# Kernel optimization log

Hardware: AMD Instinct MI355X
Metric: run time of the kernel (lower is better)

## Reference

```python
import jax, jax.numpy as jnp
import numpy as np

DIM = 1024
Q_HEADS = 16
KV_HEADS = 4
DIM_HEAD = DIM // Q_HEADS  # 64
SOFTCLAMP = 50.0
EPS = 1e-8


def rotate_half(x):
    x_even = x[..., ::2]
    x_odd = x[..., 1::2]
    return jnp.stack([-x_odd, x_even], axis=-1).reshape(x.shape)


def setup_inputs() -> dict:
    key = jax.random.key(0)
    ks = jax.random.split(key, 10)
    B, S = 1, 2048
    dim_q = DIM_HEAD * Q_HEADS   # 1024
    dim_kv = DIM_HEAD * KV_HEADS  # 256
    std = 0.02
    x = jax.random.normal(ks[0], (B, S, DIM), dtype=jnp.float32)
    positions = jnp.broadcast_to(jnp.arange(S, dtype=jnp.int32)[None, :], (B, S))
    # causal mask: True = disallowed (torch semantics: allowed = ~attn_mask)
    attn_mask = jnp.triu(jnp.ones((S, S), dtype=bool), k=1)
    return {
        "x": x,
        "positions": positions,
        "attn_mask": attn_mask,
        "Wq": jax.random.normal(ks[1], (DIM, dim_q), jnp.float32) * std,
        "Wk": jax.random.normal(ks[2], (DIM, dim_kv), jnp.float32) * std,
        "Wv": jax.random.normal(ks[3], (DIM, dim_kv), jnp.float32) * std,
        "Wo": jax.random.normal(ks[4], (dim_q, DIM), jnp.float32) * std,
        "Wg": jax.random.normal(ks[5], (DIM, Q_HEADS), jnp.float32) * std,
        "Wm": jax.random.normal(ks[6], (DIM, KV_HEADS), jnp.float32) * std,
        "bm": jnp.zeros((KV_HEADS,), jnp.float32),
        "Wvr": jax.random.normal(ks[7], (DIM, dim_kv), jnp.float32) * std,
        "k_scale": jnp.ones((KV_HEADS, DIM_HEAD), jnp.float32),
    }


def reference(x, positions, attn_mask, Wq, Wk, Wv, Wo, Wg, Wm, bm, Wvr, k_scale):
    b, s, _ = x.shape
    h, qh, dh = KV_HEADS, Q_HEADS, DIM_HEAD
    g = qh // h

    q = (x @ Wq).reshape(b, s, qh, dh).transpose(0, 2, 1, 3)  # [b,qh,s,dh]
    k = (x @ Wk).reshape(b, s, h, dh).transpose(0, 2, 1, 3)   # [b,h,s,dh]
    v = (x @ Wv).reshape(b, s, h, dh).transpose(0, 2, 1, 3)

    # value-residual gating: v = lerp(v, residual_v, mix)
    residual_v = (x @ Wvr).reshape(b, s, h, dh).transpose(0, 2, 1, 3)
    mix = jax.nn.sigmoid(x @ Wm + bm).transpose(0, 2, 1)[..., None]  # [b,h,s,1]
    v = v + mix * (residual_v - v)

    # multi-head RMSNorm on k
    rms = jnp.sqrt(jnp.mean(k * k, axis=-1, keepdims=True) + EPS)
    k = k / rms * k_scale[None, :, None, :]

    # rotary embeddings (identical for all heads -> broadcast over head dim)
    inv_freq = 1.0 / (10000.0 ** (jnp.arange(0, dh, 2, dtype=jnp.float32) / dh))
    freqs = positions.astype(jnp.float32)[..., None] * inv_freq  # [b,s,dh/2]
    cos = jnp.repeat(jnp.cos(freqs), 2, axis=-1)[:, None, :, :]  # [b,1,s,dh]
    sin = jnp.repeat(jnp.sin(freqs), 2, axis=-1)[:, None, :, :]
    q = q * cos + rotate_half(q) * sin
    k = k * cos + rotate_half(k) * sin

    # grouped-query attention with softclamped scores
    scale = dh ** -0.5
    qg = q.reshape(b, h, g, s, dh)
    sim = jnp.einsum('bhgqd,bhkd->bhgqk', qg, k) * scale
    sim = jnp.tanh(sim / SOFTCLAMP) * SOFTCLAMP
    allowed = ~attn_mask  # [s,s]
    sim = jnp.where(allowed[None, None, None, :, :], sim, jnp.finfo(sim.dtype).min)
    attn = jax.nn.softmax(sim, axis=-1)
    out = jnp.einsum('bhgqk,bhkd->bhgqd', attn, v).reshape(b, qh, s, dh)

    # per-query-head sigmoid gates
    gates = jax.nn.sigmoid(x @ Wg).transpose(0, 2, 1)[..., None]  # [b,qh,s,1]
    out = out * gates

    out = out.transpose(0, 2, 1, 3).reshape(b, s, qh * dh)
    return out @ Wo
```

## Files before the change

### kernel.cpp

```cpp
#include <hip/hip_runtime.h>
#include <hip/hip_bf16.h>
#include <math.h>

typedef unsigned short u16;
typedef unsigned int u32;
typedef __attribute__((ext_vector_type(8))) __bf16 bf16x8;
typedef __attribute__((ext_vector_type(4))) float f32x4;

__device__ inline u16 f2bf(float f) {
  u32 b = __float_as_uint(f);
  b += 0x7FFFu + ((b >> 16) & 1u);
  return (u16)(b >> 16);
}
__device__ inline float bf2f(u16 b) { return __uint_as_float((u32)b << 16); }

__global__ __launch_bounds__(256) void cvt_bf16_k(
    const float* __restrict__ in, u16* __restrict__ out) {
  int i = (blockIdx.x * 256 + threadIdx.x) * 8;
  float4 v0 = *(const float4*)&in[i];
  float4 v1 = *(const float4*)&in[i + 4];
  uint4 pk;
  pk.x = (u32)f2bf(v0.x) | ((u32)f2bf(v0.y) << 16);
  pk.y = (u32)f2bf(v0.z) | ((u32)f2bf(v0.w) << 16);
  pk.z = (u32)f2bf(v1.x) | ((u32)f2bf(v1.y) << 16);
  pk.w = (u32)f2bf(v1.z) | ((u32)f2bf(v1.w) << 16);
  *(uint4*)&out[i] = pk;
}

__global__ __launch_bounds__(256) void prep_w_k(
    const float* __restrict__ Wq, const float* __restrict__ Wk,
    const float* __restrict__ Wv, const float* __restrict__ Wvr,
    const float* __restrict__ Wo, const float* __restrict__ Wg,
    const float* __restrict__ Wm, u16* __restrict__ WallT,
    u16* __restrict__ WoT) {
  __shared__ float tile[32][33];
  int k0 = blockIdx.x * 32;
  int ybl = blockIdx.y;
  int tx = threadIdx.x, ty = threadIdx.y;
  const float* src;
  int scol, sN, drow;
  u16* dst;
  if (ybl >= 60) {
    src = Wo; scol = (ybl - 60) * 32; sN = 1024; dst = WoT; drow = scol;
  } else {
    int n0 = ybl * 32;
    if (n0 >= 1792) {
#pragma unroll
      for (int j = 0; j < 4; ++j) {
        int n = n0 + ty * 4 + j, j2 = n - 1792, k = k0 + tx;
        float val = (j2 < 16) ? Wg[(size_t)k * 16 + j2]
                  : (j2 < 20) ? Wm[(size_t)k * 4 + (j2 - 16)] : 0.f;
        WallT[(size_t)n * 1024 + k] = f2bf(val);
      }
      return;
    }
    dst = WallT; drow = n0;
    if (n0 < 1024) { src = Wq; scol = n0; sN = 1024; }
    else if (n0 < 1280) { src = Wk; scol = n0 - 1024; sN = 256; }
    else if (n0 < 1536) { src = Wv; scol = n0 - 1280; sN = 256; }
    else { src = Wvr; scol = n0 - 1536; sN = 256; }
  }
#pragma unroll
  for (int j = 0; j < 4; ++j)
    tile[ty * 4 + j][tx] = src[(size_t)(k0 + ty * 4 + j) * sN + scol + tx];
  __syncthreads();
#pragma unroll
  for (int j = 0; j < 4; ++j)
    dst[(size_t)(drow + ty * 4 + j) * 1024 + k0 + tx] = f2bf(tile[tx][ty * 4 + j]);
}

__global__ __launch_bounds__(256) void rope_tab_k(
    const int* __restrict__ positions, float* __restrict__ tab) {
  int idx = blockIdx.x * 256 + threadIdx.x;
  int s = idx >> 5, f = idx & 31;
  float inv = __expf(-(float)f * (9.210340371976184f / 32.f));
  float ang = (float)positions[s] * inv;
  tab[(size_t)s * 64 + f] = cosf(ang);
  tab[(size_t)s * 64 + 32 + f] = sinf(ang);
}

template <int BM, bool BF16_OUT>
__global__ __launch_bounds__(512) void gemm_bf16_k(
    const u16* __restrict__ A, const u16* __restrict__ Bt, void* __restrict__ Cv,
    int M, int N, int K) {
  constexpr int MI = BM / 32;
  __shared__ __align__(16) u16 As[BM * 64];
  __shared__ __align__(16) u16 Bs[128 * 64];
  int tid = threadIdx.x;
  int w = tid >> 6, l = tid & 63;
  int wr = w >> 2, wc = w & 3;
  int lr = l & 15, lg = l >> 4;
  int m0 = blockIdx.y * BM, n0 = blockIdx.x * 128;
  f32x4 zero = {0.f, 0.f, 0.f, 0.f};
  f32x4 acc[MI][2];
#pragma unroll
  for (int mi = 0; mi < MI; ++mi)
#pragma unroll
    for (int ni = 0; ni < 2; ++ni) acc[mi][ni] = zero;

  for (int kt = 0; kt < K; kt += 64) {
    __syncthreads();
#pragma unroll
    for (int c = 0; c < BM * 64 / (8 * 512); ++c) {
      int idx = c * 512 + tid;
      int row = idx >> 3, k0 = (idx & 7) * 8;
      *(uint4*)&As[row * 64 + k0] =
          *(const uint4*)&A[(size_t)(m0 + row) * K + kt + k0];
    }
#pragma unroll
    for (int c = 0; c < 2; ++c) {
      int idx = c * 512 + tid;
      int row = idx >> 3, k0 = (idx & 7) * 8;
      *(uint4*)&Bs[row * 64 + k0] =
          *(const uint4*)&Bt[(size_t)(n0 + row) * K + kt + k0];
    }
    __syncthreads();
#pragma unroll
    for (int kw = 0; kw < 2; ++kw) {
      bf16x8 af[MI], bfr[2];
#pragma unroll
      for (int mi = 0; mi < MI; ++mi)
        af[mi] = *(const bf16x8*)&As[(wr * (BM / 2) + mi * 16 + lr) * 64 + kw * 32 + lg * 8];
#pragma unroll
      for (int ni = 0; ni < 2; ++ni)
        bfr[ni] = *(const bf16x8*)&Bs[(wc * 32 + ni * 16 + lr) * 64 + kw * 32 + lg * 8];
#pragma unroll
      for (int mi = 0; mi < MI; ++mi)
#pragma unroll
        for (int ni = 0; ni < 2; ++ni)
          acc[mi][ni] = __builtin_amdgcn_mfma_f32_16x16x32_bf16(
              af[mi], bfr[ni], acc[mi][ni], 0, 0, 0);
    }
  }
#pragma unroll
  for (int mi = 0; mi < MI; ++mi)
#pragma unroll
    for (int ni = 0; ni < 2; ++ni)
#pragma unroll
      for (int r = 0; r < 4; ++r) {
        int row = m0 + wr * (BM / 2) + mi * 16 + lg * 4 + r;
        int col = n0 + wc * 32 + ni * 16 + lr;
        if (BF16_OUT)
          ((u16*)Cv)[(size_t)row * N + col] = f2bf(acc[mi][ni][r]);
        else
          ((float*)Cv)[(size_t)row * N + col] = acc[mi][ni][r];
      }
}

__global__ __launch_bounds__(256) void postproc_k(
    const float* __restrict__ bm, const float* __restrict__ ksc,
    const float* __restrict__ rtab, u16* __restrict__ qkvrb,
    u16* __restrict__ kb, u16* __restrict__ vb, float* __restrict__ g_out) {
  int s = blockIdx.x, tid = threadIdx.x;
  int lane = tid & 63, w = tid >> 6;
  u16* row = qkvrb + (size_t)s * 1920;
  const float* tr = rtab + (size_t)s * 64;
  if (tid < 16)
    g_out[s * 16 + tid] = 1.f / (1.f + __expf(-bf2f(row[1792 + tid])));
  int h = w, d = lane;
  float c = tr[d >> 1], sn = tr[32 + (d >> 1)];
  {
    float mixv = 1.f / (1.f + __expf(-(bf2f(row[1808 + h]) + bm[h])));
    float vv = bf2f(row[1280 + h * 64 + d]);
    float rv = bf2f(row[1536 + h * 64 + d]);
    vb[((size_t)h * 2048 + s) * 64 + d] = f2bf(vv + mixv * (rv - vv));
  }
  {
    float kv = bf2f(row[1024 + h * 64 + d]);
    float ss = kv * kv;
#pragma unroll
    for (int off = 32; off > 0; off >>= 1) ss += __shfl_xor(ss, off);
    float rms = sqrtf(ss * (1.f / 64.f) + 1e-8f);
    float kn = kv / rms * ksc[h * 64 + d];
    float partner = __shfl_xor(kn, 1);
    kb[((size_t)h * 2048 + s) * 64 + d] =
        f2bf((d & 1) ? fmaf(kn, c, partner * sn) : fmaf(kn, c, -partner * sn));
  }
#pragma unroll
  for (int r = 0; r < 4; ++r) {
    int e = r * 256 + tid;
    int dq = e & 63;
    float cq = tr[dq >> 1], sq = tr[32 + (dq >> 1)];
    float qv = bf2f(row[e]);
    float partner = __shfl_xor(qv, 1);
    float qr = (e & 1) ? fmaf(qv, cq, partner * sq) : fmaf(qv, cq, -partner * sq);
    row[e] = f2bf(qr * 0.125f);
  }
}

#define TPAD 66
__global__ __launch_bounds__(256) void vtrans_k(const u16* __restrict__ vb,
                                               u16* __restrict__ vtb) {
  __shared__ u16 tile[64 * TPAD];
  int h = blockIdx.y, s0 = blockIdx.x * 64;
  int t = threadIdx.x;
  {
    int r = t >> 2, cb = (t & 3) * 16;
    const u16* src = vb + ((size_t)h * 2048 + s0 + r) * 64 + cb;
    *(uint4*)&tile[r * TPAD + cb] = *(const uint4*)src;
    *(uint4*)&tile[r * TPAD + cb + 8] = *(const uint4*)(src + 8);
  }
  __syncthreads();
  int d = t >> 2, sb = (t & 3) * 16;
  u16 vals[16];
#pragma unroll
  for (int j = 0; j < 16; ++j) vals[j] = tile[(sb + j) * TPAD + d];
  uint4 a, b;
  a.x = (u32)vals[0] | ((u32)vals[1] << 16);
  a.y = (u32)vals[2] | ((u32)vals[3] << 16);
  a.z = (u32)vals[4] | ((u32)vals[5] << 16);
  a.w = (u32)vals[6] | ((u32)vals[7] << 16);
  b.x = (u32)vals[8] | ((u32)vals[9] << 16);
  b.y = (u32)vals[10] | ((u32)vals[11] << 16);
  b.z = (u32)vals[12] | ((u32)vals[13] << 16);
  b.w = (u32)vals[14] | ((u32)vals[15] << 16);
  u16* dst = vtb + ((size_t)h * 64 + d) * 2048 + s0 + sb;
  *(uint4*)dst = a;
  *(uint4*)(dst + 8) = b;
}

#define KPAD 72
__global__ __launch_bounds__(256) void attn_k(
    const u16* __restrict__ qkvrb, const u16* __restrict__ kb,
    const u16* __restrict__ vtb, const float* __restrict__ g,
    u16* __restrict__ aob) {
  __shared__ __align__(16) u16 Ks[64 * KPAD];
  __shared__ __align__(16) u16 Vt[64 * KPAD];
  int head = blockIdx.x, hkv = head >> 2;
  int by = blockIdx.y;
  int rb = (by < 16) ? (31 - by) : (by - 16);
  int row0 = rb * 64;
  int tid = threadIdx.x;
  int wi = tid >> 6, l = tid & 63;
  int lr = l & 15, lg = l >> 4;
  int skey = tid >> 2, sdb = (tid & 3) * 16;
  f32x4 zero = {0.f, 0.f, 0.f, 0.f};
  const float C1 = 0.057707801635558534f;
  const float C2 = -144.26950408889634f;
  const u16* qrow = qkvrb + (size_t)(row0 + wi * 16 + lr) * 1920 + head * 64;
  bf16x8 qf0 = *(const bf16x8*)&qrow[lg * 8];
  bf16x8 qf1 = *(const bf16x8*)&qrow[32 + lg * 8];
  f32x4 acc_o[4];
#pragma unroll
  for (int nd = 0; nd < 4; ++nd) acc_o[nd] = zero;
  float l_part = 0.f;
  int qglob = row0 + wi * 16 + lr;
  int src_a = lr + (lg & 1) * 32, src_b = src_a + 16;
  uint4 rk0, rk1, rv0, rv1;
  {
    const u16* kp = kb + ((size_t)hkv * 2048 + skey) * 64 + sdb;
    rk0 = *(const uint4*)kp;
    rk1 = *(const uint4*)(kp + 8);
    const u16* vp = vtb + ((size_t)(hkv * 64 + skey)) * 2048 + sdb;
    rv0 = *(const uint4*)vp;
    rv1 = *(const uint4*)(vp + 8);
  }
#pragma unroll 1
  for (int c = 0; c <= rb; ++c) {
    *(uint4*)&Ks[skey * KPAD + sdb] = rk0;
    *(uint4*)&Ks[skey * KPAD + sdb + 8] = rk1;
    *(uint4*)&Vt[skey * KPAD + sdb] = rv0;
    *(uint4*)&Vt[skey * KPAD + sdb + 8] = rv1;
    __syncthreads();
    if (c < rb) {
      int nb = (c + 1) * 64;
      const u16* kp = kb + ((size_t)hkv * 2048 + nb + skey) * 64 + sdb;
      rk0 = *(const uint4*)kp;
      rk1 = *(const uint4*)(kp + 8);
      const u16* vp = vtb + ((size_t)(hkv * 64 + skey)) * 2048 + nb + sdb;
      rv0 = *(const uint4*)vp;
      rv1 = *(const uint4*)(vp + 8);
    }
    int kbase = c * 64;
    __builtin_amdgcn_s_setprio(1);
    f32x4 sa[4];
#pragma unroll
    for (int ni = 0; ni < 4; ++ni) {
      bf16x8 a0 = *(const bf16x8*)&Ks[(ni * 16 + lr) * KPAD + lg * 8];
      bf16x8 a1 = *(const bf16x8*)&Ks[(ni * 16 + lr) * KPAD + 32 + lg * 8];
      f32x4 t = __builtin_amdgcn_mfma_f32_16x16x32_bf16(a0, qf0, zero, 0, 0, 0);
      sa[ni] = __builtin_amdgcn_mfma_f32_16x16x32_bf16(a1, qf1, t, 0, 0, 0);
    }
    bool diag = (c == rb);
    u32 pkw[4][2];
#pragma unroll
    for (int ni = 0; ni < 4; ++ni) {
      float pv[4];
#pragma unroll
      for (int r = 0; r < 4; ++r) {
        float sv = sa[ni][r];
        float e = __builtin_amdgcn_exp2f(sv * C1);
        float p = __builtin_amdgcn_exp2f(C2 * __builtin_amdgcn_rcpf(e + 1.f));
        if (diag && (kbase + ni * 16 + lg * 4 + r) > qglob) p = 0.f;
        pv[r] = p;
        l_part += p;
      }
      asm("v_cvt_pk_bf16_f32 %0, %1, %2" : "=v"(pkw[ni][0]) : "v"(pv[0]), "v"(pv[1]));
      asm("v_cvt_pk_bf16_f32 %0, %1, %2" : "=v"(pkw[ni][1]) : "v"(pv[2]), "v"(pv[3]));
    }
    union { u32 w[4]; bf16x8 v; } pf0, pf1;
    {
      u32 t0[4], t1[4], t2[4], t3[4];
#define GATHER(T, NI)                          \
      T[0] = __shfl((int)pkw[NI][0], src_a);   \
      T[1] = __shfl((int)pkw[NI][1], src_a);   \
      T[2] = __shfl((int)pkw[NI][0], src_b);   \
      T[3] = __shfl((int)pkw[NI][1], src_b);
      GATHER(t0, 0)
      GATHER(t1, 1)
      GATHER(t2, 2)
      GATHER(t3, 3)
#undef GATHER
      bool hi = (lg & 2) != 0;
#pragma unroll
      for (int kq = 0; kq < 4; ++kq) {
        pf0.w[kq] = hi ? t1[kq] : t0[kq];
        pf1.w[kq] = hi ? t3[kq] : t2[kq];
      }
    }
#pragma unroll
    for (int nd = 0; nd < 4; ++nd) {
      bf16x8 v0 = *(const bf16x8*)&Vt[(nd * 16 + lr) * KPAD + lg * 8];
      bf16x8 v1 = *(const bf16x8*)&Vt[(nd * 16 + lr) * KPAD + 32 + lg * 8];
      acc_o[nd] = __builtin_amdgcn_mfma_f32_16x16x32_bf16(pf0.v, v0, acc_o[nd], 0, 0, 0);
      acc_o[nd] = __builtin_amdgcn_mfma_f32_16x16x32_bf16(pf1.v, v1, acc_o[nd], 0, 0, 0);
    }
    __builtin_amdgcn_s_setprio(0);
    __syncthreads();
  }
  l_part += __shfl_xor(l_part, 16);
  l_part += __shfl_xor(l_part, 32);
#pragma unroll
  for (int r = 0; r < 4; ++r) {
    int row = row0 + wi * 16 + lg * 4 + r;
    float lv = __shfl(l_part, lg * 4 + r);
    float sc = g[row * 16 + head] * __builtin_amdgcn_rcpf(lv);
#pragma unroll
    for (int nd = 0; nd < 4; ++nd)
      aob[(size_t)row * 1024 + head * 64 + nd * 16 + lr] =
          f2bf(acc_o[nd][r] * sc);
  }
}

extern "C" void kernel_launch(void* const* d_in, const int* in_sizes, int n_in,
                              void* d_out, int out_size, void* d_ws,
                              size_t ws_size, hipStream_t stream) {
  const float* x = (const float*)d_in[0];
  const int* positions = (const int*)d_in[1];
  const float* Wq = (const float*)d_in[3];
  const float* Wk = (const float*)d_in[4];
  const float* Wv = (const float*)d_in[5];
  const float* Wo = (const float*)d_in[6];
  const float* Wg = (const float*)d_in[7];
  const float* Wm = (const float*)d_in[8];
  const float* bm = (const float*)d_in[9];
  const float* Wvr = (const float*)d_in[10];
  const float* ksc = (const float*)d_in[11];
  float* out = (float*)d_out;

  u16* xb = (u16*)d_ws;
  u16* WallT = xb + (size_t)2048 * 1024;
  u16* WoT = WallT + (size_t)1920 * 1024;
  u16* qkvrb = WoT + (size_t)1024 * 1024;
  u16* kbuf = qkvrb + (size_t)2048 * 1920;
  u16* vbuf = kbuf + (size_t)4 * 2048 * 64;
  u16* vtb = vbuf + (size_t)4 * 2048 * 64;
  float* gbuf = (float*)(vtb + (size_t)4 * 2048 * 64);
  float* rtab = gbuf + (size_t)2048 * 16;
  u16* aob = xb;

  cvt_bf16_k<<<1024, 256, 0, stream>>>(x, xb);
  prep_w_k<<<dim3(32, 92), dim3(32, 8), 0, stream>>>(Wq, Wk, Wv, Wvr, Wo, Wg,
                                                     Wm, WallT, WoT);
  rope_tab_k<<<256, 256, 0, stream>>>(positions, rtab);
  gemm_bf16_k<128, true><<<dim3(15, 16), 512, 0, stream>>>(xb, WallT, qkvrb,
                                                           2048, 1920, 1024);
  postproc_k<<<2048, 256, 0, stream>>>(bm, ksc, rtab, qkvrb, kbuf, vbuf, gbuf);
  vtrans_k<<<dim3(32, 4), 256, 0, stream>>>(vbuf, vtb);
  attn_k<<<dim3(16, 32), 256, 0, stream>>>(qkvrb, kbuf, vtb, gbuf, aob);
  gemm_bf16_k<64, false><<<dim3(8, 32), 512, 0, stream>>>(aob, WoT, out, 2048,
                                                          1024, 1024);
}
```

Before: 109.0 us.

## Split attention KV loop across two wave groups and pair causal row blocks per workgroup

The attention kernel now runs 512 threads per block, with two groups of four waves each taking alternate KV chunks for the same query rows. The partial outputs and row sums are merged through shared memory before the final write. Each block also handles a long and a short causal row block in sequence, which halves the grid and balances work across blocks. This shortens the serial KV chain per row block, at the cost of extra barriers, a shared-memory reduction, and idle iterations when one group has no chunk left.

```diff
diff --git a/kernel.cpp b/kernel.cpp
--- a/kernel.cpp
+++ b/kernel.cpp
@@ -220,125 +220,152 @@
 }
 
 #define KPAD 72
-__global__ __launch_bounds__(256) void attn_k(
+__global__ __launch_bounds__(512) void attn_k(
     const u16* __restrict__ qkvrb, const u16* __restrict__ kb,
     const u16* __restrict__ vtb, const float* __restrict__ g,
     u16* __restrict__ aob) {
-  __shared__ __align__(16) u16 Ks[64 * KPAD];
-  __shared__ __align__(16) u16 Vt[64 * KPAD];
+  __shared__ __align__(16) u16 smem[18432];
   int head = blockIdx.x, hkv = head >> 2;
-  int by = blockIdx.y;
-  int rb = (by < 16) ? (31 - by) : (by - 16);
-  int row0 = rb * 64;
   int tid = threadIdx.x;
-  int wi = tid >> 6, l = tid & 63;
+  int w = tid >> 6, l = tid & 63;
+  int grp = w >> 2, wi = w & 3;
   int lr = l & 15, lg = l >> 4;
-  int skey = tid >> 2, sdb = (tid & 3) * 16;
+  int gtid = wi * 64 + l;
+  int skey = gtid >> 2, sdb = (gtid & 3) * 16;
+  u16* Ks = smem + grp * 9216;
+  u16* Vt = smem + grp * 9216 + 4608;
+  float* mbuf = (float*)smem;
   f32x4 zero = {0.f, 0.f, 0.f, 0.f};
   const float C1 = 0.057707801635558534f;
   const float C2 = -144.26950408889634f;
-  const u16* qrow = qkvrb + (size_t)(row0 + wi * 16 + lr) * 1920 + head * 64;
-  bf16x8 qf0 = *(const bf16x8*)&qrow[lg * 8];
-  bf16x8 qf1 = *(const bf16x8*)&qrow[32 + lg * 8];
-  f32x4 acc_o[4];
-#pragma unroll
-  for (int nd = 0; nd < 4; ++nd) acc_o[nd] = zero;
-  float l_part = 0.f;
-  int qglob = row0 + wi * 16 + lr;
   int src_a = lr + (lg & 1) * 32, src_b = src_a + 16;
-  uint4 rk0, rk1, rv0, rv1;
-  {
-    const u16* kp = kb + ((size_t)hkv * 2048 + skey) * 64 + sdb;
-    rk0 = *(const uint4*)kp;
-    rk1 = *(const uint4*)(kp + 8);
-    const u16* vp = vtb + ((size_t)(hkv * 64 + skey)) * 2048 + sdb;
-    rv0 = *(const uint4*)vp;
-    rv1 = *(const uint4*)(vp + 8);
-  }
+  bool hi = (lg & 2) != 0;
 #pragma unroll 1
-  for (int c = 0; c <= rb; ++c) {
-    *(uint4*)&Ks[skey * KPAD + sdb] = rk0;
-    *(uint4*)&Ks[skey * KPAD + sdb + 8] = rk1;
-    *(uint4*)&Vt[skey * KPAD + sdb] = rv0;
-    *(uint4*)&Vt[skey * KPAD + sdb + 8] = rv1;
-    __syncthreads();
-    if (c < rb) {
-      int nb = (c + 1) * 64;
-      const u16* kp = kb + ((size_t)hkv * 2048 + nb + skey) * 64 + sdb;
+  for (int half = 0; half < 2; ++half) {
+    int rb = half ? (int)blockIdx.y : (31 - (int)blockIdx.y);
+    int row0 = rb * 64;
+    const u16* qrow = qkvrb + (size_t)(row0 + wi * 16 + lr) * 1920 + head * 64;
+    bf16x8 qf0 = *(const bf16x8*)&qrow[lg * 8];
+    bf16x8 qf1 = *(const bf16x8*)&qrow[32 + lg * 8];
+    f32x4 acc_o[4];
+#pragma unroll
+    for (int nd = 0; nd < 4; ++nd) acc_o[nd] = zero;
+    float l_part = 0.f;
+    int qglob = row0 + wi * 16 + lr;
+    int c = grp;
+    uint4 rk0, rk1, rv0, rv1;
+    if (c <= rb) {
+      const u16* kp = kb + ((size_t)hkv * 2048 + c * 64 + skey) * 64 + sdb;
       rk0 = *(const uint4*)kp;
       rk1 = *(const uint4*)(kp + 8);
-      const u16* vp = vtb + ((size_t)(hkv * 64 + skey)) * 2048 + nb + sdb;
+      const u16* vp = vtb + ((size_t)(hkv * 64 + skey)) * 2048 + c * 64 + sdb;
       rv0 = *(const uint4*)vp;
       rv1 = *(const uint4*)(vp + 8);
     }
-    int kbase = c * 64;
-    __builtin_amdgcn_s_setprio(1);
-    f32x4 sa[4];
-#pragma unroll
-    for (int ni = 0; ni < 4; ++ni) {
-      bf16x8 a0 = *(const bf16x8*)&Ks[(ni * 16 + lr) * KPAD + lg * 8];
-      bf16x8 a1 = *(const bf16x8*)&Ks[(ni * 16 + lr) * KPAD + 32 + lg * 8];
-      f32x4 t = __builtin_amdgcn_mfma_f32_16x16x32_bf16(a0, qf0, zero, 0, 0, 0);
-      sa[ni] = __builtin_amdgcn_mfma_f32_16x16x32_bf16(a1, qf1, t, 0, 0, 0);
-    }
-    bool diag = (c == rb);
-    u32 pkw[4][2];
-#pragma unroll
-    for (int ni = 0; ni < 4; ++ni) {
-      float pv[4];
+    int nmax = (rb >> 1) + 1;
+#pragma unroll 1
+    for (int i = 0; i < nmax; ++i, c += 2) {
+      bool valid = (c <= rb);
+      if (valid) {
+        *(uint4*)&Ks[skey * KPAD + sdb] = rk0;
+        *(uint4*)&Ks[skey * KPAD + sdb + 8] = rk1;
+        *(uint4*)&Vt[skey * KPAD + sdb] = rv0;
+        *(uint4*)&Vt[skey * KPAD + sdb + 8] = rv1;
+      }
+      __syncthreads();
+      if (valid && c + 2 <= rb) {
+        int nb = (c + 2) * 64;
+        const u16* kp = kb + ((size_t)hkv * 2048 + nb + skey) * 64 + sdb;
+        rk0 = *(const uint4*)kp;
+        rk1 = *(const uint4*)(kp + 8);
+        const u16* vp = vtb + ((size_t)(hkv * 64 + skey)) * 2048 + nb + sdb;
+        rv0 = *(const uint4*)vp;
+        rv1 = *(const uint4*)(vp + 8);
+      }
+      if (valid) {
+        int kbase = c * 64;
+        __builtin_amdgcn_s_setprio(1);
+        f32x4 sa[4];
+#pragma unroll
+        for (int ni = 0; ni < 4; ++ni) {
+          bf16x8 a0 = *(const bf16x8*)&Ks[(ni * 16 + lr) * KPAD + lg * 8];
+          bf16x8 a1 = *(const bf16x8*)&Ks[(ni * 16 + lr) * KPAD + 32 + lg * 8];
+          f32x4 t = __builtin_amdgcn_mfma_f32_16x16x32_bf16(a0, qf0, zero, 0, 0, 0);
+          sa[ni] = __builtin_amdgcn_mfma_f32_16x16x32_bf16(a1, qf1, t, 0, 0, 0);
+        }
+        bool diag = (c == rb);
+        u32 pkw[4][2];
+#pragma unroll
+        for (int ni = 0; ni < 4; ++ni) {
+          float pv[4];
+#pragma unroll
+          for (int r = 0; r < 4; ++r) {
+            float sv = sa[ni][r];
+            float e = __builtin_amdgcn_exp2f(sv * C1);
+            float p = __builtin_amdgcn_exp2f(C2 * __builtin_amdgcn_rcpf(e + 1.f));
+            if (diag && (kbase + ni * 16 + lg * 4 + r) > qglob) p = 0.f;
+            pv[r] = p;
+            l_part += p;
+          }
+          asm("v_cvt_pk_bf16_f32 %0, %1, %2" : "=v"(pkw[ni][0]) : "v"(pv[0]), "v"(pv[1]));
+          asm("v_cvt_pk_bf16_f32 %0, %1, %2" : "=v"(pkw[ni][1]) : "v"(pv[2]), "v"(pv[3]));
+        }
+        union { u32 w[4]; bf16x8 v; } pf0, pf1;
+        {
+          u32 t0[4], t1[4], t2[4], t3[4];
+#define GATHER(T, NI)                          \
+          T[0] = __shfl((int)pkw[NI][0], src_a);   \
+          T[1] = __shfl((int)pkw[NI][1], src_a);   \
+          T[2] = __shfl((int)pkw[NI][0], src_b);   \
+          T[3] = __shfl((int)pkw[NI][1], src_b);
+          GATHER(t0, 0)
+          GATHER(t1, 1)
+          GATHER(t2, 2)
+          GATHER(t3, 3)
+#undef GATHER
+#pragma unroll
+          for (int kq = 0; kq < 4; ++kq) {
+            pf0.w[kq] = hi ? t1[kq] : t0[kq];
+            pf1.w[kq] = hi ? t3[kq] : t2[kq];
+          }
+        }
+#pragma unroll
+        for (int nd = 0; nd < 4; ++nd) {
+          bf16x8 v0 = *(const bf16x8*)&Vt[(nd * 16 + lr) * KPAD + lg * 8];
+          bf16x8 v1 = *(const bf16x8*)&Vt[(nd * 16 + lr) * KPAD + 32 + lg * 8];
+          acc_o[nd] = __builtin_amdgcn_mfma_f32_16x16x32_bf16(pf0.v, v0, acc_o[nd], 0, 0, 0);
+          acc_o[nd] = __builtin_amdgcn_mfma_f32_16x16x32_bf16(pf1.v, v1, acc_o[nd], 0, 0, 0);
+        }
+        __builtin_amdgcn_s_setprio(0);
+      }
+      __syncthreads();
+    }
+    l_part += __shfl_xor(l_part, 16);
+    l_part += __shfl_xor(l_part, 32);
+    if (grp == 1) {
+      float* mb = mbuf + (size_t)gtid * 17;
+#pragma unroll
+      for (int nd = 0; nd < 4; ++nd)
+#pragma unroll
+        for (int r = 0; r < 4; ++r) mb[nd * 4 + r] = acc_o[nd][r];
+      mb[16] = l_part;
+    }
+    __syncthreads();
+    if (grp == 0) {
+      const float* mb = mbuf + (size_t)gtid * 17;
+      float lt = l_part + mb[16];
 #pragma unroll
       for (int r = 0; r < 4; ++r) {
-        float sv = sa[ni][r];
-        float e = __builtin_amdgcn_exp2f(sv * C1);
-        float p = __builtin_amdgcn_exp2f(C2 * __builtin_amdgcn_rcpf(e + 1.f));
-        if (diag && (kbase + ni * 16 + lg * 4 + r) > qglob) p = 0.f;
-        pv[r] = p;
-        l_part += p;
-      }
-      asm("v_cvt_pk_bf16_f32 %0, %1, %2" : "=v"(pkw[ni][0]) : "v"(pv[0]), "v"(pv[1]));
-      asm("v_cvt_pk_bf16_f32 %0, %1, %2" : "=v"(pkw[ni][1]) : "v"(pv[2]), "v"(pv[3]));
-    }
-    union { u32 w[4]; bf16x8 v; } pf0, pf1;
-    {
-      u32 t0[4], t1[4], t2[4], t3[4];
-#define GATHER(T, NI)                          \
-      T[0] = __shfl((int)pkw[NI][0], src_a);   \
-      T[1] = __shfl((int)pkw[NI][1], src_a);   \
-      T[2] = __shfl((int)pkw[NI][0], src_b);   \
-      T[3] = __shfl((int)pkw[NI][1], src_b);
-      GATHER(t0, 0)
-      GATHER(t1, 1)
-      GATHER(t2, 2)
-      GATHER(t3, 3)
-#undef GATHER
-      bool hi = (lg & 2) != 0;
-#pragma unroll
-      for (int kq = 0; kq < 4; ++kq) {
-        pf0.w[kq] = hi ? t1[kq] : t0[kq];
-        pf1.w[kq] = hi ? t3[kq] : t2[kq];
-      }
-    }
-#pragma unroll
-    for (int nd = 0; nd < 4; ++nd) {
-      bf16x8 v0 = *(const bf16x8*)&Vt[(nd * 16 + lr) * KPAD + lg * 8];
-      bf16x8 v1 = *(const bf16x8*)&Vt[(nd * 16 + lr) * KPAD + 32 + lg * 8];
-      acc_o[nd] = __builtin_amdgcn_mfma_f32_16x16x32_bf16(pf0.v, v0, acc_o[nd], 0, 0, 0);
-      acc_o[nd] = __builtin_amdgcn_mfma_f32_16x16x32_bf16(pf1.v, v1, acc_o[nd], 0, 0, 0);
-    }
-    __builtin_amdgcn_s_setprio(0);
+        int row = row0 + wi * 16 + lg * 4 + r;
+        float lv = __shfl(lt, lg * 4 + r);
+        float sc = g[row * 16 + head] * __builtin_amdgcn_rcpf(lv);
+#pragma unroll
+        for (int nd = 0; nd < 4; ++nd)
+          aob[(size_t)row * 1024 + head * 64 + nd * 16 + lr] =
+              f2bf((acc_o[nd][r] + mb[nd * 4 + r]) * sc);
+      }
+    }
     __syncthreads();
-  }
-  l_part += __shfl_xor(l_part, 16);
-  l_part += __shfl_xor(l_part, 32);
-#pragma unroll
-  for (int r = 0; r < 4; ++r) {
-    int row = row0 + wi * 16 + lg * 4 + r;
-    float lv = __shfl(l_part, lg * 4 + r);
-    float sc = g[row * 16 + head] * __builtin_amdgcn_rcpf(lv);
-#pragma unroll
-    for (int nd = 0; nd < 4; ++nd)
-      aob[(size_t)row * 1024 + head * 64 + nd * 16 + lr] =
-          f2bf(acc_o[nd][r] * sc);
   }
 }
 
@@ -377,7 +404,7 @@
                                                            2048, 1920, 1024);
   postproc_k<<<2048, 256, 0, stream>>>(bm, ksc, rtab, qkvrb, kbuf, vbuf, gbuf);
   vtrans_k<<<dim3(32, 4), 256, 0, stream>>>(vbuf, vtb);
-  attn_k<<<dim3(16, 32), 256, 0, stream>>>(qkvrb, kbuf, vtb, gbuf, aob);
+  attn_k<<<dim3(16, 16), 512, 0, stream>>>(qkvrb, kbuf, vtb, gbuf, aob);
   gemm_bf16_k<64, false><<<dim3(8, 32), 512, 0, stream>>>(aob, WoT, out, 2048,
                                                           1024, 1024);
 }
```

New measurement: 106.8 us. 2.0% less time.
